# Kernel optimization log

Measured on AMD Instinct MI355X. Metric: run time of the kernel, lower is better.

## Reference

```python
import jax, jax.numpy as jnp
import numpy as np

B, C, H, W = 2, 512, 64, 64
HEADS, DHEAD = 8, 64
HID = HEADS * DHEAD  # 512
GROUPS = 32
EPS = 1e-5


def setup_inputs() -> dict:
    key = jax.random.key(0)
    ks = jax.random.split(key, 10)
    w_scale = 0.02
    return {
        "x": jax.random.normal(ks[0], (B, C, H, W), dtype=jnp.float32),
        "gamma": jnp.ones((C,), dtype=jnp.float32),
        "beta": jnp.zeros((C,), dtype=jnp.float32),
        "wq": jax.random.normal(ks[1], (HID, C), dtype=jnp.float32) * w_scale,
        "bq": jax.random.normal(ks[2], (HID,), dtype=jnp.float32) * w_scale,
        "wk": jax.random.normal(ks[3], (HID, C), dtype=jnp.float32) * w_scale,
        "bk": jax.random.normal(ks[4], (HID,), dtype=jnp.float32) * w_scale,
        "wv": jax.random.normal(ks[5], (HID, C), dtype=jnp.float32) * w_scale,
        "bv": jax.random.normal(ks[6], (HID,), dtype=jnp.float32) * w_scale,
        "wo": jax.random.normal(ks[7], (C, HID), dtype=jnp.float32) * w_scale,
        "bo": jax.random.normal(ks[8], (C,), dtype=jnp.float32) * w_scale,
    }


def _group_norm(x, gamma, beta):
    b, c, h, w = x.shape
    xg = x.reshape(b, GROUPS, c // GROUPS, h * w)
    mu = jnp.mean(xg, axis=(2, 3), keepdims=True)
    var = jnp.var(xg, axis=(2, 3), keepdims=True)
    xn = (xg - mu) * jax.lax.rsqrt(var + EPS)
    xn = xn.reshape(b, c, h, w)
    return xn * gamma[None, :, None, None] + beta[None, :, None, None]


def reference(x, gamma, beta, wq, bq, wk, bk, wv, bv, wo, bo):
    b, c, h, w = x.shape
    n = h * w
    # norm + flatten spatial; embedding=None -> self-attention on normed x
    xn = _group_norm(x, gamma, beta).reshape(b, c, n)
    # 1x1 Conv1d projections == channel matmuls
    q = jnp.einsum('oc,bcn->bon', wq, xn) + bq[None, :, None]
    k = jnp.einsum('oc,bcn->bon', wk, xn) + bk[None, :, None]
    v = jnp.einsum('oc,bcn->bon', wv, xn) + bv[None, :, None]
    scale = DHEAD ** (-0.25)  # applied to BOTH q and k, as in source
    qh = q.reshape(b, HEADS, DHEAD, n) * scale
    kh = k.reshape(b, HEADS, DHEAD, n) * scale
    vh = v.reshape(b, HEADS, DHEAD, n)
    # full NxN attention (the materialized score matrix targeted for kernel work)
    attn = jax.nn.softmax(jnp.einsum('bhdi,bhdj->bhij', qh, kh), axis=-1)
    out = jnp.einsum('bhij,bhdj->bhdi', attn, vh).reshape(b, HID, n)
    out = jnp.einsum('oc,bcn->bon', wo, out) + bo[None, :, None]
    out = out.reshape(b, c, h, w)
    return x + out  # in_channels == out_channels -> residual
```

## Files before the change

### kernel.cpp

```cpp
#include <hip/hip_runtime.h>
#include <math.h>

#define BB      2
#define CC      512
#define NN_TOK  4096
#define HEADS   8
#define DHEAD   64
#define HID     512
#define GROUPS  32
#define CPG     (CC / GROUPS)
#define EPS     1e-5f

typedef __bf16 bf16x8 __attribute__((ext_vector_type(8)));
typedef float  f32x4  __attribute__((ext_vector_type(4)));
typedef float  f32x16 __attribute__((ext_vector_type(16)));
typedef int    i32x8  __attribute__((ext_vector_type(8)));

static __device__ __forceinline__ unsigned short f2bf(float f) {
  __bf16 h = (__bf16)f;
  return __builtin_bit_cast(unsigned short, h);
}
static __device__ __forceinline__ float bf2f(unsigned short u) {
  unsigned v = (unsigned)u << 16;
  return __builtin_bit_cast(float, v);
}
static __device__ __forceinline__ unsigned pk_fp8x4(float a, float b, float c, float d) {
  int lo = __builtin_amdgcn_cvt_pk_fp8_f32(a, b, 0, false);
  return (unsigned)__builtin_amdgcn_cvt_pk_fp8_f32(c, d, lo, true);
}
static __device__ __forceinline__ unsigned char f2fp8(float a) {
  return (unsigned char)(__builtin_amdgcn_cvt_pk_fp8_f32(a, a, 0, false) & 0xff);
}
static __device__ __forceinline__ long mklong(unsigned lo, unsigned hi) {
  return (long)(((unsigned long long)hi << 32) | lo);
}
static __device__ __forceinline__ i32x8 ld_frag32(const unsigned char* p) {
  union { i32x8 v; long l[4]; } u;
  u.l[0] = *(const long*)(p + 0);
  u.l[1] = *(const long*)(p + 8);
  u.l[2] = *(const long*)(p + 16);
  u.l[3] = *(const long*)(p + 24);
  return u.v;
}
#define SC_ONE 0x7F7F7F7F
#define QKV_WS 32.0f
#define QKV_WS_INV 0.03125f
#define WO_WS 16.0f
#define WO_WS_INV 0.0625f

__global__ __launch_bounds__(256) void gn_stats_wconv_kernel(
    const float* __restrict__ x, float2* __restrict__ part,
    const float* __restrict__ wq, const float* __restrict__ wk,
    const float* __restrict__ wv, const float* __restrict__ wo,
    unsigned char* __restrict__ wq8, unsigned char* __restrict__ wk8,
    unsigned char* __restrict__ wv8, unsigned char* __restrict__ wo8) {
  int blk = blockIdx.x;
  int t = threadIdx.x;
  {
    int wsel = blk >> 6;
    int off = (blk & 63) * 4096 + t * 16;
    const float* s = (wsel == 0) ? wq : (wsel == 1) ? wk : (wsel == 2) ? wv : wo;
    unsigned char* d = (wsel == 0) ? wq8 : (wsel == 1) ? wk8 : (wsel == 2) ? wv8 : wo8;
    float sc = (wsel < 3) ? QKV_WS : WO_WS;
    #pragma unroll
    for (int i = 0; i < 4; ++i) {
      float4 a = *(const float4*)&s[off + i * 4];
      *(unsigned*)&d[off + i * 4] =
          pk_fp8x4(a.x * sc, a.y * sc, a.z * sc, a.w * sc);
    }
  }
  const float4* __restrict__ x4 = (const float4*)(x + (size_t)blk * 16384);
  float s = 0.f, ss = 0.f;
  #pragma unroll
  for (int i = 0; i < 16; ++i) {
    float4 v = x4[t + i * 256];
    s  += v.x + v.y + v.z + v.w;
    ss += v.x * v.x + v.y * v.y + v.z * v.z + v.w * v.w;
  }
  #pragma unroll
  for (int off = 32; off >= 1; off >>= 1) {
    s  += __shfl_down(s, off, 64);
    ss += __shfl_down(ss, off, 64);
  }
  __shared__ float rs[4], rss[4];
  int wid = t >> 6, lane = t & 63;
  if (lane == 0) { rs[wid] = s; rss[wid] = ss; }
  __syncthreads();
  if (t == 0) {
    float2 o;
    o.x = rs[0] + rs[1] + rs[2] + rs[3];
    o.y = rss[0] + rss[1] + rss[2] + rss[3];
    part[blk] = o;
  }
}

__global__ __launch_bounds__(256) void gn_norm_t_kernel(
    const float* __restrict__ x, const float* __restrict__ gamma,
    const float* __restrict__ beta, const float2* __restrict__ part,
    unsigned char* __restrict__ xnT8) {
  __shared__ __align__(16) unsigned short lds[64 * 72];
  __shared__ float mu4[4], rs4[4];
  int b = blockIdx.z;
  int t0 = blockIdx.x * 64, c0 = blockIdx.y * 64;
  int t = threadIdx.x;
  if (t < 4) {
    int g = (c0 >> 4) + t;
    int gi = b * GROUPS + g;
    float2 p0 = part[gi * 4 + 0], p1 = part[gi * 4 + 1];
    float2 p2 = part[gi * 4 + 2], p3 = part[gi * 4 + 3];
    float S = p0.x + p1.x + p2.x + p3.x;
    float SS = p0.y + p1.y + p2.y + p3.y;
    const float inv_n = 1.0f / (float)(CPG * NN_TOK);
    float mu = S * inv_n;
    float var = SS * inv_n - mu * mu;
    mu4[t] = mu;
    rs4[t] = rsqrtf(var + EPS);
  }
  __syncthreads();
  const float* __restrict__ xb = x + (size_t)b * CC * NN_TOK;
  #pragma unroll
  for (int i = 0; i < 4; ++i) {
    int f = t + i * 256;
    int row = f >> 4, c16 = f & 15;
    int c = c0 + row;
    float ga = gamma[c] * rs4[row >> 4];
    float be = beta[c] - mu4[row >> 4] * ga;
    float4 v = *(const float4*)&xb[(size_t)c * NN_TOK + t0 + c16 * 4];
    ushort4 pk;
    pk.x = f2bf(v.x * ga + be); pk.y = f2bf(v.y * ga + be);
    pk.z = f2bf(v.z * ga + be); pk.w = f2bf(v.w * ga + be);
    *(ushort4*)&lds[row * 72 + c16 * 4] = pk;
  }
  __syncthreads();
  unsigned char* __restrict__ ob = xnT8 + (size_t)b * NN_TOK * CC;
  #pragma unroll
  for (int i = 0; i < 2; ++i) {
    int f = t + i * 256;
    int row = f >> 3, ch = f & 7;
    float v0 = bf2f(lds[(ch * 8 + 0) * 72 + row]);
    float v1 = bf2f(lds[(ch * 8 + 1) * 72 + row]);
    float v2 = bf2f(lds[(ch * 8 + 2) * 72 + row]);
    float v3 = bf2f(lds[(ch * 8 + 3) * 72 + row]);
    float v4 = bf2f(lds[(ch * 8 + 4) * 72 + row]);
    float v5 = bf2f(lds[(ch * 8 + 5) * 72 + row]);
    float v6 = bf2f(lds[(ch * 8 + 6) * 72 + row]);
    float v7 = bf2f(lds[(ch * 8 + 7) * 72 + row]);
    unsigned lo = pk_fp8x4(v0, v1, v2, v3);
    unsigned hi = pk_fp8x4(v4, v5, v6, v7);
    *(uint2*)&ob[(size_t)(t0 + row) * CC + c0 + ch * 8] = make_uint2(lo, hi);
  }
}

__global__ __launch_bounds__(256, 3) void qkv_gemm_kernel(
    const unsigned char* __restrict__ xnT8,
    const unsigned char* __restrict__ wq8, const unsigned char* __restrict__ wk8,
    const unsigned char* __restrict__ wv8,
    const float* __restrict__ bq, const float* __restrict__ bk,
    const float* __restrict__ bv,
    unsigned char* __restrict__ qT8, unsigned char* __restrict__ kT8,
    unsigned char* __restrict__ vB8) {
  __shared__ __align__(16) unsigned char As8[128 * 72];
  __shared__ __align__(16) unsigned char Bs8[128 * 72];
  int b = blockIdx.z;
  int y = blockIdx.y;
  int which = y >> 2, yl = y & 3;
  const unsigned char* __restrict__ W =
      (which == 0) ? wq8 : (which == 1) ? wk8 : wv8;
  const float* __restrict__ bias = (which == 0) ? bq : (which == 1) ? bk : bv;
  int m0 = yl * 128;
  int n0 = blockIdx.x * 128;
  const unsigned char* __restrict__ Bsrc = xnT8 + (size_t)b * NN_TOK * CC;
  int t = threadIdx.x, w = t >> 6, lane = t & 63;
  int wm = (w >> 1) * 64, wn = (w & 1) * 64;
  int l31 = lane & 31, q1h = lane >> 5;

  const f32x16 z16 = {0,0,0,0,0,0,0,0,0,0,0,0,0,0,0,0};
  f32x16 acc[2][2];
  #pragma unroll
  for (int mt = 0; mt < 2; ++mt)
    #pragma unroll
    for (int nt = 0; nt < 2; ++nt) acc[mt][nt] = z16;

  for (int kc = 0; kc < CC; kc += 64) {
    __syncthreads();
    #pragma unroll
    for (int i = 0; i < 2; ++i) {
      int idx = t + i * 256;
      int row = idx >> 2, ch = idx & 3;
      uint4 a = *(const uint4*)&W[(size_t)(m0 + row) * CC + kc + ch * 16];
      unsigned char* ad = &As8[row * 72 + ch * 16];
      *(uint2*)ad = make_uint2(a.x, a.y);
      *(uint2*)(ad + 8) = make_uint2(a.z, a.w);
      uint4 bb = *(const uint4*)&Bsrc[(size_t)(n0 + row) * CC + kc + ch * 16];
      unsigned char* bd = &Bs8[row * 72 + ch * 16];
      *(uint2*)bd = make_uint2(bb.x, bb.y);
      *(uint2*)(bd + 8) = make_uint2(bb.z, bb.w);
    }
    __syncthreads();
    i32x8 af[2], bfm[2];
    #pragma unroll
    for (int i = 0; i < 2; ++i) {
      af[i]  = ld_frag32(&As8[(wm + i * 32 + l31) * 72 + q1h * 32]);
      bfm[i] = ld_frag32(&Bs8[(wn + i * 32 + l31) * 72 + q1h * 32]);
    }
    #pragma unroll
    for (int mt = 0; mt < 2; ++mt)
      #pragma unroll
      for (int nt = 0; nt < 2; ++nt)
        acc[mt][nt] = __builtin_amdgcn_mfma_scale_f32_32x32x64_f8f6f4(
            af[mt], bfm[nt], acc[mt][nt], 0, 0, 0, SC_ONE, 0, SC_ONE);
  }
  __syncthreads();

  if (which < 2) {
    const float sc = (which == 0) ? 0.18033688011112043f : 1.0f;
    unsigned char* __restrict__ dstT = (which == 0) ? qT8 : kT8;
    unsigned char* buf = As8 + w * 2560;
    int h = (m0 + wm) >> 6;
    const size_t hbase = (size_t)(b * HEADS + h) * NN_TOK;
    #pragma unroll
    for (int p = 0; p < 2; ++p) {
      #pragma unroll
      for (int mt = 0; mt < 2; ++mt) {
        #pragma unroll
        for (int g = 0; g < 4; ++g) {
          float4 bv4 = *(const float4*)&bias[m0 + wm + mt * 32 + g * 8 + q1h * 4];
          f32x16 a = acc[mt][p];
          unsigned pk = pk_fp8x4((a[4 * g + 0] * QKV_WS_INV + bv4.x) * sc,
                                 (a[4 * g + 1] * QKV_WS_INV + bv4.y) * sc,
                                 (a[4 * g + 2] * QKV_WS_INV + bv4.z) * sc,
                                 (a[4 * g + 3] * QKV_WS_INV + bv4.w) * sc);
          *(unsigned*)&buf[l31 * 80 + mt * 32 + g * 8 + q1h * 4] = pk;
        }
      }
      #pragma unroll
      for (int it = 0; it < 2; ++it) {
        int idx = it * 64 + lane;
        int row = idx >> 2, ch = idx & 3;
        int tok = n0 + wn + p * 32 + row;
        *(uint4*)&dstT[(hbase + tok) * DHEAD + ch * 16] =
            *(const uint4*)&buf[row * 80 + ch * 16];
      }
      __syncthreads();
    }
  } else {
    unsigned char* __restrict__ dst = vB8 + (size_t)b * HID * NN_TOK;
    #pragma unroll
    for (int mt = 0; mt < 2; ++mt) {
      #pragma unroll
      for (int g = 0; g < 4; ++g) {
        float4 bv4 = *(const float4*)&bias[m0 + wm + mt * 32 + g * 8 + q1h * 4];
        float bvr[4] = {bv4.x, bv4.y, bv4.z, bv4.w};
        #pragma unroll
        for (int nt = 0; nt < 2; ++nt) {
          int tok = n0 + wn + nt * 32 + l31;
          #pragma unroll
          for (int r = 0; r < 4; ++r) {
            int m = m0 + wm + mt * 32 + g * 8 + q1h * 4 + r;
            dst[(size_t)m * NN_TOK + tok] =
                f2fp8(acc[mt][nt][4 * g + r] * QKV_WS_INV + bvr[r]);
          }
        }
      }
    }
  }
}

__global__ __launch_bounds__(256) void outproj_kernel(
    const unsigned char* __restrict__ aoT8, const unsigned char* __restrict__ wo8,
    const float* __restrict__ bo, const float* __restrict__ x,
    float* __restrict__ out) {
  __shared__ __align__(16) unsigned char As8[128 * 80];
  __shared__ __align__(16) unsigned char Bs8[64 * 80];
  int b = blockIdx.z;
  int m0 = blockIdx.y * 128;
  int n0 = blockIdx.x * 64;
  const unsigned char* __restrict__ Bsrc = aoT8 + (size_t)b * NN_TOK * HID;
  int t = threadIdx.x, w = t >> 6, lane = t & 63;
  int wm = (w & 1) * 64, wn = (w >> 1) * 32;
  int l31 = lane & 31, q1h = lane >> 5;

  const f32x16 z16 = {0,0,0,0,0,0,0,0,0,0,0,0,0,0,0,0};
  f32x16 acc[2];
  acc[0] = z16; acc[1] = z16;

  for (int kc = 0; kc < HID; kc += 64) {
    __syncthreads();
    #pragma unroll
    for (int i = 0; i < 2; ++i) {
      int f = t + i * 256;
      int row = f >> 2, ch = f & 3;
      *(uint4*)&As8[row * 80 + ch * 16] =
          *(const uint4*)&wo8[(size_t)(m0 + row) * HID + kc + ch * 16];
    }
    {
      int row = t >> 2, ch = t & 3;
      *(uint4*)&Bs8[row * 80 + ch * 16] =
          *(const uint4*)&Bsrc[(size_t)(n0 + row) * HID + kc + ch * 16];
    }
    __syncthreads();
    i32x8 bfm = ld_frag32(&Bs8[(wn + l31) * 80 + q1h * 32]);
    #pragma unroll
    for (int mt = 0; mt < 2; ++mt) {
      i32x8 af = ld_frag32(&As8[(wm + mt * 32 + l31) * 80 + q1h * 32]);
      acc[mt] = __builtin_amdgcn_mfma_scale_f32_32x32x64_f8f6f4(
          af, bfm, acc[mt], 0, 0, 0, SC_ONE, 0, SC_ONE);
    }
  }

  const float* __restrict__ xb = x + (size_t)b * CC * NN_TOK;
  float* __restrict__ ob = out + (size_t)b * CC * NN_TOK;
  int tok = n0 + wn + l31;
  #pragma unroll
  for (int mt = 0; mt < 2; ++mt) {
    #pragma unroll
    for (int g = 0; g < 4; ++g) {
      float4 bv4 = *(const float4*)&bo[m0 + wm + mt * 32 + g * 8 + q1h * 4];
      float bvr[4] = {bv4.x, bv4.y, bv4.z, bv4.w};
      #pragma unroll
      for (int r = 0; r < 4; ++r) {
        int m = m0 + wm + mt * 32 + g * 8 + q1h * 4 + r;
        size_t off = (size_t)m * NN_TOK + tok;
        ob[off] = acc[mt][4 * g + r] * WO_WS_INV + bvr[r] + xb[off];
      }
    }
  }
}

__global__ __launch_bounds__(512, 4) void attn_mfma_kernel(
    const unsigned char* __restrict__ qT8, const unsigned char* __restrict__ kT8,
    const unsigned char* __restrict__ vv8, unsigned char* __restrict__ aoT8) {
  __shared__ __align__(16) unsigned char kvs[4 * 4608];
  __shared__ __align__(16) unsigned char st8[4 * 32 * 80];
  __shared__ float lbuf[128];
  unsigned char* ks8 = kvs;
  unsigned char* vs8 = kvs + 2 * 4608;
  int bh = blockIdx.y;
  int b = bh >> 3, h = bh & 7;
  int i0 = blockIdx.x * 128;
  const size_t hb = (size_t)bh * NN_TOK;
  const unsigned char* __restrict__ qtg = qT8 + hb * DHEAD;
  const unsigned char* __restrict__ ktg = kT8 + hb * DHEAD;
  const unsigned char* __restrict__ vg  = vv8 + hb * DHEAD;
  int t = threadIdx.x;
  int w = t >> 6, lane = t & 63, l31 = lane & 31, q1h = lane >> 5;
  int strip = w & 3, parity = w >> 2;
  int iw = i0 + strip * 32;

  const unsigned char* qrow = qtg + (size_t)(iw + l31) * DHEAD + q1h * 32;
  uint4 qv0 = *(const uint4*)(qrow);
  uint4 qv1 = *(const uint4*)(qrow + 16);
  i32x8 qf = {(int)qv0.x, (int)qv0.y, (int)qv0.z, (int)qv0.w,
              (int)qv1.x, (int)qv1.y, (int)qv1.z, (int)qv1.w};
  i32x8 ones;
  #pragma unroll
  for (int i = 0; i < 8; ++i) ones[i] = 0x38383838;

  const f32x16 z16 = {0,0,0,0,0,0,0,0,0,0,0,0,0,0,0,0};
  f32x16 o0 = z16, o1 = z16, lacc = z16;
  const unsigned char* __restrict__ ksw = ks8 + parity * 4608;
  const unsigned char* __restrict__ vsw = vs8 + parity * 4608;

  for (int rt = 0; rt < NN_TOK / 128; ++rt) {
    int j0 = rt * 128;
    __syncthreads();
    {
      int jr = t >> 2, ch = t & 3;
      int ktile = jr >> 6, krow = jr & 63;
      uint4 kx = *(const uint4*)&ktg[(size_t)(j0 + jr) * DHEAD + ch * 16];
      unsigned char* kd = &ks8[ktile * 4608 + krow * 72 + ch * 16];
      *(uint2*)kd = make_uint2(kx.x, kx.y);
      *(uint2*)(kd + 8) = make_uint2(kx.z, kx.w);
      int vtile = t >> 8, vrr = (t >> 2) & 63, vch = t & 3;
      uint4 vx = *(const uint4*)&vg[(size_t)vrr * NN_TOK + j0 + vtile * 64 + vch * 16];
      unsigned char* vd = &vs8[vtile * 4608 + vrr * 72 + vch * 16];
      *(uint2*)vd = make_uint2(vx.x, vx.y);
      *(uint2*)(vd + 8) = make_uint2(vx.z, vx.w);
    }
    __syncthreads();

    i32x8 ka0 = ld_frag32(&ksw[l31 * 72 + q1h * 32]);
    i32x8 ka1 = ld_frag32(&ksw[(32 + l31) * 72 + q1h * 32]);
    f32x16 s0 = __builtin_amdgcn_mfma_scale_f32_32x32x64_f8f6f4(
        ka0, qf, z16, 0, 0, 0, SC_ONE, 0, SC_ONE);
    f32x16 s1 = __builtin_amdgcn_mfma_scale_f32_32x32x64_f8f6f4(
        ka1, qf, z16, 0, 0, 0, SC_ONE, 0, SC_ONE);

    unsigned pk4[8];
    #pragma unroll
    for (int g = 0; g < 4; ++g) {
      float p0 = __builtin_amdgcn_exp2f(s0[4 * g + 0]);
      float p1 = __builtin_amdgcn_exp2f(s0[4 * g + 1]);
      float p2 = __builtin_amdgcn_exp2f(s0[4 * g + 2]);
      float p3 = __builtin_amdgcn_exp2f(s0[4 * g + 3]);
      pk4[g] = pk_fp8x4(p0, p1, p2, p3);
    }
    #pragma unroll
    for (int g = 0; g < 4; ++g) {
      float p0 = __builtin_amdgcn_exp2f(s1[4 * g + 0]);
      float p1 = __builtin_amdgcn_exp2f(s1[4 * g + 1]);
      float p2 = __builtin_amdgcn_exp2f(s1[4 * g + 2]);
      float p3 = __builtin_amdgcn_exp2f(s1[4 * g + 3]);
      pk4[4 + g] = pk_fp8x4(p0, p1, p2, p3);
    }

    i32x8 pb;
    #pragma unroll
    for (int g = 0; g < 4; ++g) {
      unsigned send = q1h ? pk4[g] : pk4[4 + g];
      unsigned got = (unsigned)__shfl_xor((int)send, 32);
      pb[2 * g]     = (int)(q1h ? got : pk4[g]);
      pb[2 * g + 1] = (int)(q1h ? pk4[4 + g] : got);
    }

    i32x8 va0 = ld_frag32(&vsw[l31 * 72 + q1h * 32]);
    i32x8 va1 = ld_frag32(&vsw[(32 + l31) * 72 + q1h * 32]);
    o0 = __builtin_amdgcn_mfma_scale_f32_32x32x64_f8f6f4(
        va0, pb, o0, 0, 0, 0, SC_ONE, 0, SC_ONE);
    o1 = __builtin_amdgcn_mfma_scale_f32_32x32x64_f8f6f4(
        va1, pb, o1, 0, 0, 0, SC_ONE, 0, SC_ONE);
    lacc = __builtin_amdgcn_mfma_scale_f32_32x32x64_f8f6f4(
        ones, pb, lacc, 0, 0, 0, SC_ONE, 0, SC_ONE);
  }
  float lrun = lacc[0];

  float* obuf = (float*)kvs;
  __syncthreads();
  if (parity == 1) {
    #pragma unroll
    for (int r = 0; r < 16; ++r) {
      int d = (r & 3) + 8 * (r >> 2) + 4 * q1h;
      obuf[strip * 1024 + d * 32 + l31] = o0[r];
    }
    if (q1h == 0) lbuf[strip * 32 + l31] = lrun;
  }
  __syncthreads();
  if (parity == 0) {
    lrun += lbuf[strip * 32 + l31];
    #pragma unroll
    for (int r = 0; r < 16; ++r) {
      int d = (r & 3) + 8 * (r >> 2) + 4 * q1h;
      o0[r] += obuf[strip * 1024 + d * 32 + l31];
    }
  }
  __syncthreads();
  if (parity == 1) {
    #pragma unroll
    for (int r = 0; r < 16; ++r) {
      int d = (r & 3) + 8 * (r >> 2) + 4 * q1h;
      obuf[strip * 1024 + d * 32 + l31] = o1[r];
    }
  }
  __syncthreads();
  if (parity == 0) {
    #pragma unroll
    for (int r = 0; r < 16; ++r) {
      int d = (r & 3) + 8 * (r >> 2) + 4 * q1h;
      o1[r] += obuf[strip * 1024 + d * 32 + l31];
    }
    float inv = 1.0f / lrun;
    unsigned char* stw = st8 + strip * 2560;
    #pragma unroll
    for (int dm = 0; dm < 2; ++dm) {
      #pragma unroll
      for (int g = 0; g < 4; ++g) {
        float v0 = ((dm == 0) ? o0[4 * g + 0] : o1[4 * g + 0]) * inv;
        float v1 = ((dm == 0) ? o0[4 * g + 1] : o1[4 * g + 1]) * inv;
        float v2 = ((dm == 0) ? o0[4 * g + 2] : o1[4 * g + 2]) * inv;
        float v3 = ((dm == 0) ? o0[4 * g + 3] : o1[4 * g + 3]) * inv;
        *(unsigned*)&stw[l31 * 80 + dm * 32 + g * 8 + q1h * 4] =
            pk_fp8x4(v0, v1, v2, v3);
      }
    }
    const size_t obase = (size_t)b * NN_TOK;
    #pragma unroll
    for (int it = 0; it < 4; ++it) {
      int idx = it * 64 + lane;
      int row = idx >> 3, ch = idx & 7;
      int tok = iw + row;
      *(uint2*)&aoT8[(obase + tok) * HID + h * DHEAD + ch * 8] =
          *(const uint2*)&stw[row * 80 + ch * 8];
    }
  }
}

extern "C" void kernel_launch(void* const* d_in, const int* in_sizes, int n_in,
                              void* d_out, int out_size, void* d_ws, size_t ws_size,
                              hipStream_t stream) {
  const float* x     = (const float*)d_in[0];
  const float* gamma = (const float*)d_in[1];
  const float* beta  = (const float*)d_in[2];
  const float* wq    = (const float*)d_in[3];
  const float* bq    = (const float*)d_in[4];
  const float* wk    = (const float*)d_in[5];
  const float* bk    = (const float*)d_in[6];
  const float* wv    = (const float*)d_in[7];
  const float* bv    = (const float*)d_in[8];
  const float* wo    = (const float*)d_in[9];
  const float* bo    = (const float*)d_in[10];
  float* out = (float*)d_out;

  const size_t SZ = (size_t)BB * CC * NN_TOK;
  const size_t WZ = (size_t)CC * HID;
  unsigned char* xnT8 = (unsigned char*)d_ws;
  unsigned char* qT8  = xnT8 + SZ;
  unsigned char* kT8  = qT8 + SZ;
  unsigned char* vB8  = kT8 + SZ;
  unsigned char* aoT8 = vB8 + SZ;
  unsigned char* wq8  = aoT8 + SZ;
  unsigned char* wk8  = wq8 + WZ;
  unsigned char* wv8  = wk8 + WZ;
  unsigned char* wo8  = wv8 + WZ;
  float2* gnpart = (float2*)(wo8 + WZ);

  gn_stats_wconv_kernel<<<dim3(256), dim3(256), 0, stream>>>(
      x, gnpart, wq, wk, wv, wo, wq8, wk8, wv8, wo8);

  gn_norm_t_kernel<<<dim3(NN_TOK / 64, CC / 64, BB), dim3(256), 0, stream>>>(
      x, gamma, beta, gnpart, xnT8);

  qkv_gemm_kernel<<<dim3(NN_TOK / 128, 12, BB), dim3(256), 0, stream>>>(
      xnT8, wq8, wk8, wv8, bq, bk, bv, qT8, kT8, vB8);

  attn_mfma_kernel<<<dim3(NN_TOK / 128, BB * HEADS), dim3(512), 0, stream>>>(
      qT8, kT8, vB8, aoT8);

  outproj_kernel<<<dim3(NN_TOK / 64, CC / 128, BB), dim3(256), 0, stream>>>(
      aoT8, wo8, bo, x, out);
}
```

Baseline: 174.6 us.

## Double-buffer LDS tiles with register prefetch in GEMM and attention loops

In the QKV GEMM, out-projection GEMM and attention kernels, the next K-chunk's global loads are now issued into registers right after the current tile is stored to shared memory. The loads then overlap with the MFMA compute of the current iteration. Shared memory is double-buffered so the write for the next iteration does not race with readers of the current one. This costs twice the LDS and extra live registers, which could lower occupancy, especially for the attention kernel declared with launch bounds (512,4).

New measurement: 176.1 us. No clear change (+0.9%).

```diff
diff --git a/kernel.cpp b/kernel.cpp
--- a/kernel.cpp
+++ b/kernel.cpp
@@ -30,9 +30,6 @@
 }
 static __device__ __forceinline__ unsigned char f2fp8(float a) {
   return (unsigned char)(__builtin_amdgcn_cvt_pk_fp8_f32(a, a, 0, false) & 0xff);
-}
-static __device__ __forceinline__ long mklong(unsigned lo, unsigned hi) {
-  return (long)(((unsigned long long)hi << 32) | lo);
 }
 static __device__ __forceinline__ i32x8 ld_frag32(const unsigned char* p) {
   union { i32x8 v; long l[4]; } u;
@@ -159,8 +156,7 @@
     const float* __restrict__ bv,
     unsigned char* __restrict__ qT8, unsigned char* __restrict__ kT8,
     unsigned char* __restrict__ vB8) {
-  __shared__ __align__(16) unsigned char As8[128 * 72];
-  __shared__ __align__(16) unsigned char Bs8[128 * 72];
+  __shared__ __align__(16) unsigned char AB[2][2][128 * 72];
   int b = blockIdx.z;
   int y = blockIdx.y;
   int which = y >> 2, yl = y & 3;
@@ -174,6 +170,16 @@
   int wm = (w >> 1) * 64, wn = (w & 1) * 64;
   int l31 = lane & 31, q1h = lane >> 5;
 
+  int sr0 = t >> 2, sr1 = (t + 256) >> 2, sch = t & 3;
+  const unsigned char* Wa0 = &W[(size_t)(m0 + sr0) * CC + sch * 16];
+  const unsigned char* Wa1 = &W[(size_t)(m0 + sr1) * CC + sch * 16];
+  const unsigned char* Bb0 = &Bsrc[(size_t)(n0 + sr0) * CC + sch * 16];
+  const unsigned char* Bb1 = &Bsrc[(size_t)(n0 + sr1) * CC + sch * 16];
+  uint4 ra0 = *(const uint4*)(Wa0);
+  uint4 ra1 = *(const uint4*)(Wa1);
+  uint4 rb0 = *(const uint4*)(Bb0);
+  uint4 rb1 = *(const uint4*)(Bb1);
+
   const f32x16 z16 = {0,0,0,0,0,0,0,0,0,0,0,0,0,0,0,0};
   f32x16 acc[2][2];
   #pragma unroll
@@ -181,27 +187,39 @@
     #pragma unroll
     for (int nt = 0; nt < 2; ++nt) acc[mt][nt] = z16;
 
+  int cur = 0;
   for (int kc = 0; kc < CC; kc += 64) {
     __syncthreads();
+    {
+      unsigned char* As = AB[cur][0];
+      unsigned char* Bs = AB[cur][1];
+      unsigned char* ad0 = &As[sr0 * 72 + sch * 16];
+      *(uint2*)ad0 = make_uint2(ra0.x, ra0.y);
+      *(uint2*)(ad0 + 8) = make_uint2(ra0.z, ra0.w);
+      unsigned char* ad1 = &As[sr1 * 72 + sch * 16];
+      *(uint2*)ad1 = make_uint2(ra1.x, ra1.y);
+      *(uint2*)(ad1 + 8) = make_uint2(ra1.z, ra1.w);
+      unsigned char* bd0 = &Bs[sr0 * 72 + sch * 16];
+      *(uint2*)bd0 = make_uint2(rb0.x, rb0.y);
+      *(uint2*)(bd0 + 8) = make_uint2(rb0.z, rb0.w);
+      unsigned char* bd1 = &Bs[sr1 * 72 + sch * 16];
+      *(uint2*)bd1 = make_uint2(rb1.x, rb1.y);
+      *(uint2*)(bd1 + 8) = make_uint2(rb1.z, rb1.w);
+    }
+    if (kc + 64 < CC) {
+      ra0 = *(const uint4*)(Wa0 + kc + 64);
+      ra1 = *(const uint4*)(Wa1 + kc + 64);
+      rb0 = *(const uint4*)(Bb0 + kc + 64);
+      rb1 = *(const uint4*)(Bb1 + kc + 64);
+    }
+    __syncthreads();
+    const unsigned char* As = AB[cur][0];
+    const unsigned char* Bs = AB[cur][1];
+    i32x8 af[2], bfm[2];
     #pragma unroll
     for (int i = 0; i < 2; ++i) {
-      int idx = t + i * 256;
-      int row = idx >> 2, ch = idx & 3;
-      uint4 a = *(const uint4*)&W[(size_t)(m0 + row) * CC + kc + ch * 16];
-      unsigned char* ad = &As8[row * 72 + ch * 16];
-      *(uint2*)ad = make_uint2(a.x, a.y);
-      *(uint2*)(ad + 8) = make_uint2(a.z, a.w);
-      uint4 bb = *(const uint4*)&Bsrc[(size_t)(n0 + row) * CC + kc + ch * 16];
-      unsigned char* bd = &Bs8[row * 72 + ch * 16];
-      *(uint2*)bd = make_uint2(bb.x, bb.y);
-      *(uint2*)(bd + 8) = make_uint2(bb.z, bb.w);
-    }
-    __syncthreads();
-    i32x8 af[2], bfm[2];
-    #pragma unroll
-    for (int i = 0; i < 2; ++i) {
-      af[i]  = ld_frag32(&As8[(wm + i * 32 + l31) * 72 + q1h * 32]);
-      bfm[i] = ld_frag32(&Bs8[(wn + i * 32 + l31) * 72 + q1h * 32]);
+      af[i]  = ld_frag32(&As[(wm + i * 32 + l31) * 72 + q1h * 32]);
+      bfm[i] = ld_frag32(&Bs[(wn + i * 32 + l31) * 72 + q1h * 32]);
     }
     #pragma unroll
     for (int mt = 0; mt < 2; ++mt)
@@ -209,13 +227,14 @@
       for (int nt = 0; nt < 2; ++nt)
         acc[mt][nt] = __builtin_amdgcn_mfma_scale_f32_32x32x64_f8f6f4(
             af[mt], bfm[nt], acc[mt][nt], 0, 0, 0, SC_ONE, 0, SC_ONE);
+    cur ^= 1;
   }
   __syncthreads();
 
   if (which < 2) {
     const float sc = (which == 0) ? 0.18033688011112043f : 1.0f;
     unsigned char* __restrict__ dstT = (which == 0) ? qT8 : kT8;
-    unsigned char* buf = As8 + w * 2560;
+    unsigned char* buf = (unsigned char*)AB + w * 2560;
     int h = (m0 + wm) >> 6;
     const size_t hbase = (size_t)(b * HEADS + h) * NN_TOK;
     #pragma unroll
@@ -270,8 +289,8 @@
     const unsigned char* __restrict__ aoT8, const unsigned char* __restrict__ wo8,
     const float* __restrict__ bo, const float* __restrict__ x,
     float* __restrict__ out) {
-  __shared__ __align__(16) unsigned char As8[128 * 80];
-  __shared__ __align__(16) unsigned char Bs8[64 * 80];
+  __shared__ __align__(16) unsigned char As8[2][128 * 80];
+  __shared__ __align__(16) unsigned char Bs8[2][64 * 80];
   int b = blockIdx.z;
   int m0 = blockIdx.y * 128;
   int n0 = blockIdx.x * 64;
@@ -280,32 +299,38 @@
   int wm = (w & 1) * 64, wn = (w >> 1) * 32;
   int l31 = lane & 31, q1h = lane >> 5;
 
+  int ar0 = t >> 2, ar1 = (t + 256) >> 2, ach = t & 3;
+  const unsigned char* pa0 = &wo8[(size_t)(m0 + ar0) * HID + ach * 16];
+  const unsigned char* pa1 = &wo8[(size_t)(m0 + ar1) * HID + ach * 16];
+  const unsigned char* pb  = &Bsrc[(size_t)(n0 + ar0) * HID + ach * 16];
+  uint4 ra0 = *(const uint4*)(pa0);
+  uint4 ra1 = *(const uint4*)(pa1);
+  uint4 rb  = *(const uint4*)(pb);
+
   const f32x16 z16 = {0,0,0,0,0,0,0,0,0,0,0,0,0,0,0,0};
   f32x16 acc[2];
   acc[0] = z16; acc[1] = z16;
 
+  int cur = 0;
   for (int kc = 0; kc < HID; kc += 64) {
     __syncthreads();
-    #pragma unroll
-    for (int i = 0; i < 2; ++i) {
-      int f = t + i * 256;
-      int row = f >> 2, ch = f & 3;
-      *(uint4*)&As8[row * 80 + ch * 16] =
-          *(const uint4*)&wo8[(size_t)(m0 + row) * HID + kc + ch * 16];
-    }
-    {
-      int row = t >> 2, ch = t & 3;
-      *(uint4*)&Bs8[row * 80 + ch * 16] =
-          *(const uint4*)&Bsrc[(size_t)(n0 + row) * HID + kc + ch * 16];
+    *(uint4*)&As8[cur][ar0 * 80 + ach * 16] = ra0;
+    *(uint4*)&As8[cur][ar1 * 80 + ach * 16] = ra1;
+    *(uint4*)&Bs8[cur][ar0 * 80 + ach * 16] = rb;
+    if (kc + 64 < HID) {
+      ra0 = *(const uint4*)(pa0 + kc + 64);
+      ra1 = *(const uint4*)(pa1 + kc + 64);
+      rb  = *(const uint4*)(pb + kc + 64);
     }
     __syncthreads();
-    i32x8 bfm = ld_frag32(&Bs8[(wn + l31) * 80 + q1h * 32]);
+    i32x8 bfm = ld_frag32(&Bs8[cur][(wn + l31) * 80 + q1h * 32]);
     #pragma unroll
     for (int mt = 0; mt < 2; ++mt) {
-      i32x8 af = ld_frag32(&As8[(wm + mt * 32 + l31) * 80 + q1h * 32]);
+      i32x8 af = ld_frag32(&As8[cur][(wm + mt * 32 + l31) * 80 + q1h * 32]);
       acc[mt] = __builtin_amdgcn_mfma_scale_f32_32x32x64_f8f6f4(
           af, bfm, acc[mt], 0, 0, 0, SC_ONE, 0, SC_ONE);
     }
+    cur ^= 1;
   }
 
   const float* __restrict__ xb = x + (size_t)b * CC * NN_TOK;
@@ -330,11 +355,9 @@
 __global__ __launch_bounds__(512, 4) void attn_mfma_kernel(
     const unsigned char* __restrict__ qT8, const unsigned char* __restrict__ kT8,
     const unsigned char* __restrict__ vv8, unsigned char* __restrict__ aoT8) {
-  __shared__ __align__(16) unsigned char kvs[4 * 4608];
+  __shared__ __align__(16) unsigned char kvs[2 * 18432];
   __shared__ __align__(16) unsigned char st8[4 * 32 * 80];
   __shared__ float lbuf[128];
-  unsigned char* ks8 = kvs;
-  unsigned char* vs8 = kvs + 2 * 4608;
   int bh = blockIdx.y;
   int b = bh >> 3, h = bh & 7;
   int i0 = blockIdx.x * 128;
@@ -356,28 +379,39 @@
   #pragma unroll
   for (int i = 0; i < 8; ++i) ones[i] = 0x38383838;
 
+  int jr = t >> 2, ch = t & 3;
+  int ktile = jr >> 6, krow = jr & 63;
+  int vtile = t >> 8, vrr = (t >> 2) & 63, vch = t & 3;
+  const unsigned char* kga = &ktg[(size_t)jr * DHEAD + ch * 16];
+  const unsigned char* vga = &vg[(size_t)vrr * NN_TOK + vtile * 64 + vch * 16];
+  int kldso = ktile * 4608 + krow * 72 + ch * 16;
+  int vldso = 9216 + vtile * 4608 + vrr * 72 + vch * 16;
+
+  uint4 kx = *(const uint4*)(kga);
+  uint4 vx = *(const uint4*)(vga);
+
   const f32x16 z16 = {0,0,0,0,0,0,0,0,0,0,0,0,0,0,0,0};
   f32x16 o0 = z16, o1 = z16, lacc = z16;
-  const unsigned char* __restrict__ ksw = ks8 + parity * 4608;
-  const unsigned char* __restrict__ vsw = vs8 + parity * 4608;
-
+
+  int cur = 0;
   for (int rt = 0; rt < NN_TOK / 128; ++rt) {
-    int j0 = rt * 128;
     __syncthreads();
+    unsigned char* kb = kvs + cur * 18432;
     {
-      int jr = t >> 2, ch = t & 3;
-      int ktile = jr >> 6, krow = jr & 63;
-      uint4 kx = *(const uint4*)&ktg[(size_t)(j0 + jr) * DHEAD + ch * 16];
-      unsigned char* kd = &ks8[ktile * 4608 + krow * 72 + ch * 16];
+      unsigned char* kd = kb + kldso;
       *(uint2*)kd = make_uint2(kx.x, kx.y);
       *(uint2*)(kd + 8) = make_uint2(kx.z, kx.w);
-      int vtile = t >> 8, vrr = (t >> 2) & 63, vch = t & 3;
-      uint4 vx = *(const uint4*)&vg[(size_t)vrr * NN_TOK + j0 + vtile * 64 + vch * 16];
-      unsigned char* vd = &vs8[vtile * 4608 + vrr * 72 + vch * 16];
+      unsigned char* vd = kb + vldso;
       *(uint2*)vd = make_uint2(vx.x, vx.y);
       *(uint2*)(vd + 8) = make_uint2(vx.z, vx.w);
     }
+    if (rt + 1 < NN_TOK / 128) {
+      kx = *(const uint4*)(kga + (size_t)(rt + 1) * 128 * DHEAD);
+      vx = *(const uint4*)(vga + (rt + 1) * 128);
+    }
     __syncthreads();
+    const unsigned char* ksw = kb + parity * 4608;
+    const unsigned char* vsw = kb + 9216 + parity * 4608;
 
     i32x8 ka0 = ld_frag32(&ksw[l31 * 72 + q1h * 32]);
     i32x8 ka1 = ld_frag32(&ksw[(32 + l31) * 72 + q1h * 32]);
@@ -421,6 +455,7 @@
         va1, pb, o1, 0, 0, 0, SC_ONE, 0, SC_ONE);
     lacc = __builtin_amdgcn_mfma_scale_f32_32x32x64_f8f6f4(
         ones, pb, lacc, 0, 0, 0, SC_ONE, 0, SC_ONE);
+    cur ^= 1;
   }
   float lrun = lacc[0];
 
```
